# Kernel tuning notes

Measured on AMD Instinct MI355X. Metric: run time of the kernel, lower is better.

Reference implementation:

```python
import jax, jax.numpy as jnp
import numpy as np

B, D, K, H = 8192, 1024, 8, 2048


def setup_inputs() -> dict:
    key = jax.random.key(0)
    ks = jax.random.split(key, 4)
    x = jax.random.normal(ks[0], (B, D), dtype=jnp.float32)
    centroids = jax.random.normal(ks[1], (K, D), dtype=jnp.float32)
    W1 = jax.random.normal(ks[2], (K, D, H), dtype=jnp.float32) / np.sqrt(D).astype(np.float32)
    b1 = jnp.zeros((K, H), dtype=jnp.float32)
    W2 = jax.random.normal(ks[3], (K, H), dtype=jnp.float32) / np.sqrt(H).astype(np.float32)
    b2 = jnp.zeros((K,), dtype=jnp.float32)
    return {"x": x, "centroids": centroids, "W1": W1, "b1": b1, "W2": W2, "b2": b2}


def reference(x, centroids, W1, b1, W2, b2):
    # --- k-means hard routing: nearest centroid per sample (euclidean max_sim) ---
    # d2[b,k] = ||x_b||^2 - 2 x_b . c_k + ||c_k||^2  (avoid [B,K,D] blowup)
    d2 = (jnp.sum(x * x, axis=-1, keepdims=True)
          - 2.0 * (x @ centroids.T)
          + jnp.sum(centroids * centroids, axis=-1)[None, :])  # [B, K]
    cluster = jnp.argmin(d2, axis=-1)  # [B] int, hard assignment

    # --- per-expert log-likelihood heads (Einet stand-in), computed densely ---
    h = jnp.tanh(jnp.einsum("bd,kdh->kbh", x, W1) + b1[:, None, :])  # [K, B, H]
    lls = jnp.einsum("kbh,kh->kb", h, W2) + b2[:, None]              # [K, B]

    # --- combine: each sample takes the LL from its routed expert, original order ---
    lls_sorted = jnp.take_along_axis(lls.T, cluster[:, None], axis=1)[:, 0]  # [B]
    return lls_sorted
```

## Files before the change

### kernel.cpp

```cpp
#include <hip/hip_runtime.h>
#include <hip/hip_bf16.h>
#include <stdint.h>

#define B_N 8192
#define D_N 1024
#define K_N 8
#define H_N 2048

#define BM 320
#define BN 256
#define BK 64
#define NBLK 256
#define ABYTES 40960
#define BUFSZ 73728
#define RO_OFF 147456
#define PLL_OFF 148736
#define GEMM_LDS 153856

typedef unsigned int u32;
typedef unsigned short u16;
typedef __attribute__((ext_vector_type(8))) short short8;
typedef __attribute__((ext_vector_type(4))) float float4v;

struct __align__(8) us4 { u16 x, y, z, w; };

__device__ __forceinline__ u16 f2bf(float f) {
    union { float f; u32 u; } v; v.f = f;
    u32 u = v.u;
    u32 r = (u + 0x7fffu + ((u >> 16) & 1u)) >> 16;
    return (u16)r;
}

__device__ __forceinline__ float fast_tanh(float x) {
    float t = __expf(2.0f * x);
    return 1.0f - 2.0f * __builtin_amdgcn_rcpf(t + 1.0f);
}

__device__ __forceinline__ void async_copy16(void* lds, const void* g) {
    __builtin_amdgcn_global_load_lds(
        (const __attribute__((address_space(1))) void*)g,
        (__attribute__((address_space(3))) void*)lds, 16, 0, 0);
}

__global__ void route_kernel(const float* __restrict__ x,
                             const float* __restrict__ cent,
                             u16* __restrict__ xbf,
                             int* __restrict__ cluster,
                             u32* __restrict__ counts) {
    int tid = threadIdx.x;
    if (blockIdx.x == 0 && tid < K_N) counts[tid * 32] = 0;
    int wave = tid >> 6, lane = tid & 63;
    int b = blockIdx.x * 4 + wave;
    const float* xr = x + (size_t)b * D_N;

    float4 xv[4];
#pragma unroll
    for (int i = 0; i < 4; ++i)
        xv[i] = *(const float4*)(xr + i * 256 + lane * 4);

#pragma unroll
    for (int i = 0; i < 4; ++i) {
        us4 o;
        o.x = f2bf(xv[i].x); o.y = f2bf(xv[i].y);
        o.z = f2bf(xv[i].z); o.w = f2bf(xv[i].w);
        *(us4*)(xbf + (size_t)b * D_N + i * 256 + lane * 4) = o;
    }

    double acc[K_N];
#pragma unroll
    for (int k = 0; k < K_N; ++k) {
        const float* cr = cent + k * D_N;
        double s = 0.0;
#pragma unroll
        for (int i = 0; i < 4; ++i) {
            float4 cv = *(const float4*)(cr + i * 256 + lane * 4);
            double d0 = (double)xv[i].x - (double)cv.x; s += d0 * d0;
            double d1 = (double)xv[i].y - (double)cv.y; s += d1 * d1;
            double d2 = (double)xv[i].z - (double)cv.z; s += d2 * d2;
            double d3 = (double)xv[i].w - (double)cv.w; s += d3 * d3;
        }
        acc[k] = s;
    }
#pragma unroll
    for (int k = 0; k < K_N; ++k) {
        double v = acc[k];
        for (int off = 32; off; off >>= 1) v += __shfl_down(v, off);
        acc[k] = v;
    }
    if (lane == 0) {
        int best = 0; double bv = acc[0];
#pragma unroll
        for (int k = 1; k < K_N; ++k)
            if (acc[k] < bv) { bv = acc[k]; best = k; }
        cluster[b] = best;
    }
}

__global__ void scatter_kernel(const int* __restrict__ cluster,
                               u32* __restrict__ counts,
                               u32* __restrict__ idxl) {
    __shared__ u32 wcnt[4][K_N];
    __shared__ u32 gb[K_N];
    int tid = threadIdx.x;
    int b = blockIdx.x * 256 + tid;
    int lane = tid & 63, wid = tid >> 6;
    int cl = cluster[b];
    unsigned long long lower = (1ull << lane) - 1ull;
    u32 rank = 0;
#pragma unroll
    for (int k = 0; k < K_N; ++k) {
        unsigned long long mk = __ballot(cl == k);
        if (k == cl) rank = (u32)__popcll(mk & lower);
        if (lane == 0) wcnt[wid][k] = (u32)__popcll(mk);
    }
    __syncthreads();
    if (tid < K_N) {
        u32 tot = wcnt[0][tid] + wcnt[1][tid] + wcnt[2][tid] + wcnt[3][tid];
        gb[tid] = atomicAdd(&counts[tid * 32], tot);
    }
    __syncthreads();
    u32 woff = 0;
    if (wid > 0) woff += wcnt[0][cl];
    if (wid > 1) woff += wcnt[1][cl];
    if (wid > 2) woff += wcnt[2][cl];
    idxl[(size_t)cl * B_N + gb[cl] + woff + rank] = (u32)b;
}

__global__ void w1t_kernel(const float* __restrict__ w1, u16* __restrict__ w1t) {
    __shared__ float ts[64][65];
    int tid = threadIdx.x;
    int h0 = blockIdx.x * 64, d0 = blockIdx.y * 64, k = blockIdx.z;
    const float* src = w1 + ((size_t)k * D_N + d0) * H_N + h0;
#pragma unroll
    for (int i = 0; i < 4; ++i) {
        int q = i * 256 + tid;
        int r = q >> 4, c4 = (q & 15) * 4;
        float4 v = *(const float4*)(src + (size_t)r * H_N + c4);
        ts[c4 + 0][r] = v.x; ts[c4 + 1][r] = v.y;
        ts[c4 + 2][r] = v.z; ts[c4 + 3][r] = v.w;
    }
    __syncthreads();
    u16* dst = w1t + ((size_t)k * H_N + h0) * D_N + d0;
#pragma unroll
    for (int i = 0; i < 4; ++i) {
        int q = i * 256 + tid;
        int hr = q >> 4, d4 = (q & 15) * 4;
        us4 o;
        o.x = f2bf(ts[hr][d4 + 0]); o.y = f2bf(ts[hr][d4 + 1]);
        o.z = f2bf(ts[hr][d4 + 2]); o.w = f2bf(ts[hr][d4 + 3]);
        *(us4*)(dst + (size_t)hr * D_N + d4) = o;
    }
}

__global__ __launch_bounds__(512, 2) void gemm_kernel(
                            const u16* __restrict__ xbf,
                            const u16* __restrict__ w1t,
                            const float* __restrict__ b1,
                            const float* __restrict__ w2,
                            const u32* __restrict__ idxl,
                            const u32* __restrict__ counts,
                            float* __restrict__ llp) {
    extern __shared__ char lds[];
    int tid = threadIdx.x;
    int lane = tid & 63, w = tid >> 6;
    int wm = w >> 2, wn = w & 3;
    int wmbase = wm * 160;
    int l15 = lane & 15, l4 = lane >> 4;

    u32* ro = (u32*)(lds + RO_OFF);
    float* pll = (float*)(lds + PLL_OFF);

    int ntot = 0;
#pragma unroll
    for (int kk = 0; kk < K_N; ++kk)
        ntot += ((int)counts[kk * 32] + BM - 1) / BM;
    int total = ntot * 8;

    int swz = l15 & 7;
    u32 aB0 = (u32)((wmbase + l15) * 128 + (((0 + l4) ^ swz) << 4));
    u32 aB1 = (u32)((wmbase + l15) * 128 + (((4 + l4) ^ swz) << 4));
    u32 bB0 = (u32)(ABYTES + (wn * 64 + l15) * 128 + (((0 + l4) ^ swz) << 4));
    u32 bB1 = (u32)(ABYTES + (wn * 64 + l15) * 128 + (((4 + l4) ^ swz) << 4));

    const char* xb = (const char*)xbf;
    const char* wb = (const char*)w1t;

    for (int item = blockIdx.x; item < total; item += NBLK) {
        int tile = item >> 3, nc = item & 7;
        int k = 0, mt = 0, nt = 0;
#pragma unroll
        for (int kk = 0; kk < K_N; ++kk) {
            int c = (int)counts[kk * 32];
            int t = (c + BM - 1) / BM;
            if (tile >= nt && tile < nt + t) { k = kk; mt = tile - nt; }
            nt += t;
        }
        int cnt = (int)counts[k * 32];
        int rows = cnt - mt * BM; if (rows > BM) rows = BM;
        int h0 = nc * BN;

        if (tid < BM) {
            int m = mt * BM + tid;
            int mm = m < cnt ? m : cnt - 1;
            ro[tid] = idxl[(size_t)k * B_N + mm] * (u32)(D_N * 2);
        }
        __syncthreads();

        u32 srcA[5], srcB[4];
#pragma unroll
        for (int i = 0; i < 5; ++i) {
            int c = i * 512 + tid; int r = c >> 3, j = c & 7;
            srcA[i] = ro[r] + ((u32)(j ^ (r & 7)) << 4);
        }
#pragma unroll
        for (int i = 0; i < 4; ++i) {
            int c = i * 512 + tid; int r = c >> 3, j = c & 7;
            srcB[i] = ((u32)(k * H_N + h0 + r) << 11) + ((u32)(j ^ (r & 7)) << 4);
        }

        float4v acc[10][4];
#pragma unroll
        for (int mf = 0; mf < 10; ++mf)
#pragma unroll
            for (int nf = 0; nf < 4; ++nf)
                acc[mf][nf] = (float4v){0.f, 0.f, 0.f, 0.f};

#define STA(BUF, I, D) async_copy16((BUF) + (I) * 8192 + w * 1024, xb + srcA[I] + (D))
#define STB(BUF, I, D) async_copy16((BUF) + ABYTES + (I) * 8192 + w * 1024, wb + srcB[I] + (D))
#define BAR() do { asm volatile("" ::: "memory"); __builtin_amdgcn_s_barrier(); \
                   asm volatile("" ::: "memory"); } while (0)
#define LGKM0_PIN() do { asm volatile("s_waitcnt lgkmcnt(0)" ::: "memory"); \
                         __builtin_amdgcn_sched_barrier(0); } while (0)
#define MFMA_PHASE(MFB, BREG)                                                    \
    do {                                                                         \
        __builtin_amdgcn_s_setprio(1);                                           \
        _Pragma("unroll")                                                        \
        for (int i_ = 0; i_ < 5; ++i_) {                                         \
            if (wmbase + ((MFB) + i_) * 16 < rows) {                             \
                _Pragma("unroll")                                                \
                for (int nf_ = 0; nf_ < 4; ++nf_)                                \
                    acc[(MFB) + i_][nf_] = __builtin_amdgcn_mfma_f32_16x16x32_bf16( \
                        a[i_], BREG[nf_], acc[(MFB) + i_][nf_], 0, 0, 0);        \
            }                                                                    \
        }                                                                        \
        __builtin_amdgcn_s_setprio(0);                                           \
    } while (0)

        {
            char* Bp = lds;
            STA(Bp, 0, 0); STA(Bp, 1, 0); STA(Bp, 2, 0); STA(Bp, 3, 0); STA(Bp, 4, 0);
            STB(Bp, 0, 0); STB(Bp, 1, 0); STB(Bp, 2, 0); STB(Bp, 3, 0);
        }

        for (int t = 0; t < 16; ++t) {
            const char* Acur = lds + (t & 1) * BUFSZ;
            char* Bnx = lds + ((t + 1) & 1) * BUFSZ;
            u32 d = (u32)((t + 1) << 7);
            bool pre = (t < 15);
            short8 a[5], bC[4];

            asm volatile("s_waitcnt vmcnt(0)" ::: "memory");
            BAR();
#pragma unroll
            for (int nf = 0; nf < 4; ++nf)
                bC[nf] = *(const short8*)(Acur + bB0 + nf * 2048);
#pragma unroll
            for (int i = 0; i < 5; ++i)
                a[i] = *(const short8*)(Acur + aB0 + i * 2048);
            if (pre) { STB(Bnx, 0, d); STB(Bnx, 1, d); STB(Bnx, 2, d); }
            BAR();
            LGKM0_PIN();
            MFMA_PHASE(0, bC);

            BAR();
#pragma unroll
            for (int i = 0; i < 5; ++i)
                a[i] = *(const short8*)(Acur + aB0 + (5 + i) * 2048);
            if (pre) { STB(Bnx, 3, d); STA(Bnx, 0, d); STA(Bnx, 1, d); }
            BAR();
            LGKM0_PIN();
            MFMA_PHASE(5, bC);

            BAR();
#pragma unroll
            for (int nf = 0; nf < 4; ++nf)
                bC[nf] = *(const short8*)(Acur + bB1 + nf * 2048);
#pragma unroll
            for (int i = 0; i < 5; ++i)
                a[i] = *(const short8*)(Acur + aB1 + i * 2048);
            if (pre) { STA(Bnx, 2, d); STA(Bnx, 3, d); STA(Bnx, 4, d); }
            BAR();
            LGKM0_PIN();
            MFMA_PHASE(0, bC);

            BAR();
#pragma unroll
            for (int i = 0; i < 5; ++i)
                a[i] = *(const short8*)(Acur + aB1 + (5 + i) * 2048);
            BAR();
            LGKM0_PIN();
            MFMA_PHASE(5, bC);
        }

#undef STA
#undef STB
#undef BAR
#undef LGKM0_PIN
#undef MFMA_PHASE

        float w2v[4], b1v[4];
#pragma unroll
        for (int nf = 0; nf < 4; ++nf) {
            int h = h0 + wn * 64 + nf * 16 + l15;
            w2v[nf] = w2[k * H_N + h];
            b1v[nf] = b1[k * H_N + h];
        }
#pragma unroll
        for (int mf = 0; mf < 10; ++mf) {
            float rs[4] = {0.f, 0.f, 0.f, 0.f};
#pragma unroll
            for (int nf = 0; nf < 4; ++nf) {
#pragma unroll
                for (int r = 0; r < 4; ++r)
                    rs[r] += fast_tanh(acc[mf][nf][r] + b1v[nf]) * w2v[nf];
            }
#pragma unroll
            for (int r = 0; r < 4; ++r) {
                float v = rs[r];
                v += __shfl_xor(v, 8);
                v += __shfl_xor(v, 4);
                v += __shfl_xor(v, 2);
                v += __shfl_xor(v, 1);
                if (l15 == 0) pll[wn * 320 + wmbase + mf * 16 + l4 * 4 + r] = v;
            }
        }
        __syncthreads();
        if (tid < BM) {
            int m = mt * BM + tid;
            if (m < cnt) {
                u32 b = idxl[(size_t)k * B_N + m];
                llp[(size_t)nc * B_N + b] = pll[tid] + pll[320 + tid] + pll[640 + tid] + pll[960 + tid];
            }
        }
        __syncthreads();
    }
}

__global__ void combine_kernel(const float* __restrict__ llp,
                               const int* __restrict__ cluster,
                               const float* __restrict__ b2,
                               float* __restrict__ out) {
    int b = blockIdx.x * 256 + threadIdx.x;
    float s = b2[cluster[b]];
#pragma unroll
    for (int nc = 0; nc < 8; ++nc) s += llp[(size_t)nc * B_N + b];
    out[b] = s;
}

extern "C" void kernel_launch(void* const* d_in, const int* in_sizes, int n_in,
                              void* d_out, int out_size, void* d_ws, size_t ws_size,
                              hipStream_t stream) {
    const float* x    = (const float*)d_in[0];
    const float* cent = (const float*)d_in[1];
    const float* W1   = (const float*)d_in[2];
    const float* b1   = (const float*)d_in[3];
    const float* W2   = (const float*)d_in[4];
    const float* b2   = (const float*)d_in[5];
    float* out = (float*)d_out;

    char* ws = (char*)d_ws;
    u16* xbf     = (u16*)(ws + 0);
    u16* w1t     = (u16*)(ws + 16777216);
    u32* counts  = (u32*)(ws + 50331648);
    int* cluster = (int*)(ws + 50332672);
    u32* idxl    = (u32*)(ws + 50365440);
    float* llp   = (float*)(ws + 50627584);

    (void)hipFuncSetAttribute((const void*)gemm_kernel,
                              hipFuncAttributeMaxDynamicSharedMemorySize, GEMM_LDS);

    hipLaunchKernelGGL(route_kernel, dim3(B_N / 4), dim3(256), 0, stream,
                       x, cent, xbf, cluster, counts);
    hipLaunchKernelGGL(scatter_kernel, dim3(32), dim3(256), 0, stream,
                       cluster, counts, idxl);
    hipLaunchKernelGGL(w1t_kernel, dim3(H_N / 64, D_N / 64, K_N), dim3(256), 0, stream,
                       W1, w1t);
    hipLaunchKernelGGL(gemm_kernel, dim3(NBLK), dim3(512), GEMM_LDS, stream,
                       xbf, w1t, b1, W2, idxl, counts, llp);
    hipLaunchKernelGGL(combine_kernel, dim3(B_N / 256), dim3(256), 0, stream,
                       llp, cluster, b2, out);
}
```

Before: 88.53 us.

## Halve GEMM workgroup to four waves with 160x128 per-wave tiles

Shrinks the grouped GEMM workgroup from 8 waves to 4 waves, each computing a 160x128 output tile instead of 160x64. The goal is more register-level reuse of each A fragment across more B columns. It also replaces the four-phase barrier-interleaved schedule with one phase per K step: load all fragments, issue the next prefetch, run all MFMAs, then sync. The cost is a much larger per-thread footprint (80 accumulator fragments plus 36 operand vectors), which risks register spilling. Halving the waves per CU also gives less latency hiding and less overlap between copies and MFMAs.

Result: slower. 125.9 us (+42.2%).

```diff
diff --git a/kernel.cpp b/kernel.cpp
--- a/kernel.cpp
+++ b/kernel.cpp
@@ -15,7 +15,7 @@
 #define BUFSZ 73728
 #define RO_OFF 147456
 #define PLL_OFF 148736
-#define GEMM_LDS 153856
+#define GEMM_LDS 151296
 
 typedef unsigned int u32;
 typedef unsigned short u16;
@@ -152,7 +152,7 @@
     }
 }
 
-__global__ __launch_bounds__(512, 2) void gemm_kernel(
+__global__ __launch_bounds__(256, 1) void gemm_kernel(
                             const u16* __restrict__ xbf,
                             const u16* __restrict__ w1t,
                             const float* __restrict__ b1,
@@ -163,7 +163,7 @@
     extern __shared__ char lds[];
     int tid = threadIdx.x;
     int lane = tid & 63, w = tid >> 6;
-    int wm = w >> 2, wn = w & 3;
+    int wm = w >> 1, wn = w & 1;
     int wmbase = wm * 160;
     int l15 = lane & 15, l4 = lane >> 4;
 
@@ -179,8 +179,8 @@
     int swz = l15 & 7;
     u32 aB0 = (u32)((wmbase + l15) * 128 + (((0 + l4) ^ swz) << 4));
     u32 aB1 = (u32)((wmbase + l15) * 128 + (((4 + l4) ^ swz) << 4));
-    u32 bB0 = (u32)(ABYTES + (wn * 64 + l15) * 128 + (((0 + l4) ^ swz) << 4));
-    u32 bB1 = (u32)(ABYTES + (wn * 64 + l15) * 128 + (((4 + l4) ^ swz) << 4));
+    u32 bB0 = (u32)(ABYTES + (wn * 128 + l15) * 128 + (((0 + l4) ^ swz) << 4));
+    u32 bB1 = (u32)(ABYTES + (wn * 128 + l15) * 128 + (((4 + l4) ^ swz) << 4));
 
     const char* xb = (const char*)xbf;
     const char* wb = (const char*)w1t;
@@ -199,119 +199,99 @@
         int rows = cnt - mt * BM; if (rows > BM) rows = BM;
         int h0 = nc * BN;
 
-        if (tid < BM) {
-            int m = mt * BM + tid;
+#pragma unroll 2
+        for (int i = tid; i < BM; i += 256) {
+            int m = mt * BM + i;
             int mm = m < cnt ? m : cnt - 1;
-            ro[tid] = idxl[(size_t)k * B_N + mm] * (u32)(D_N * 2);
+            ro[i] = idxl[(size_t)k * B_N + mm] * (u32)(D_N * 2);
         }
         __syncthreads();
 
-        u32 srcA[5], srcB[4];
-#pragma unroll
-        for (int i = 0; i < 5; ++i) {
-            int c = i * 512 + tid; int r = c >> 3, j = c & 7;
+        u32 srcA[10], srcB[8];
+#pragma unroll
+        for (int i = 0; i < 10; ++i) {
+            int c = i * 256 + tid; int r = c >> 3, j = c & 7;
             srcA[i] = ro[r] + ((u32)(j ^ (r & 7)) << 4);
         }
 #pragma unroll
-        for (int i = 0; i < 4; ++i) {
-            int c = i * 512 + tid; int r = c >> 3, j = c & 7;
+        for (int i = 0; i < 8; ++i) {
+            int c = i * 256 + tid; int r = c >> 3, j = c & 7;
             srcB[i] = ((u32)(k * H_N + h0 + r) << 11) + ((u32)(j ^ (r & 7)) << 4);
         }
 
-        float4v acc[10][4];
+        float4v acc[10][8];
 #pragma unroll
         for (int mf = 0; mf < 10; ++mf)
 #pragma unroll
-            for (int nf = 0; nf < 4; ++nf)
+            for (int nf = 0; nf < 8; ++nf)
                 acc[mf][nf] = (float4v){0.f, 0.f, 0.f, 0.f};
-
-#define STA(BUF, I, D) async_copy16((BUF) + (I) * 8192 + w * 1024, xb + srcA[I] + (D))
-#define STB(BUF, I, D) async_copy16((BUF) + ABYTES + (I) * 8192 + w * 1024, wb + srcB[I] + (D))
-#define BAR() do { asm volatile("" ::: "memory"); __builtin_amdgcn_s_barrier(); \
-                   asm volatile("" ::: "memory"); } while (0)
-#define LGKM0_PIN() do { asm volatile("s_waitcnt lgkmcnt(0)" ::: "memory"); \
-                         __builtin_amdgcn_sched_barrier(0); } while (0)
-#define MFMA_PHASE(MFB, BREG)                                                    \
-    do {                                                                         \
-        __builtin_amdgcn_s_setprio(1);                                           \
-        _Pragma("unroll")                                                        \
-        for (int i_ = 0; i_ < 5; ++i_) {                                         \
-            if (wmbase + ((MFB) + i_) * 16 < rows) {                             \
-                _Pragma("unroll")                                                \
-                for (int nf_ = 0; nf_ < 4; ++nf_)                                \
-                    acc[(MFB) + i_][nf_] = __builtin_amdgcn_mfma_f32_16x16x32_bf16( \
-                        a[i_], BREG[nf_], acc[(MFB) + i_][nf_], 0, 0, 0);        \
-            }                                                                    \
-        }                                                                        \
-        __builtin_amdgcn_s_setprio(0);                                           \
-    } while (0)
 
         {
             char* Bp = lds;
-            STA(Bp, 0, 0); STA(Bp, 1, 0); STA(Bp, 2, 0); STA(Bp, 3, 0); STA(Bp, 4, 0);
-            STB(Bp, 0, 0); STB(Bp, 1, 0); STB(Bp, 2, 0); STB(Bp, 3, 0);
-        }
+#pragma unroll
+            for (int i = 0; i < 10; ++i)
+                async_copy16(Bp + i * 4096 + tid * 16, xb + srcA[i]);
+#pragma unroll
+            for (int i = 0; i < 8; ++i)
+                async_copy16(Bp + ABYTES + i * 4096 + tid * 16, wb + srcB[i]);
+        }
+        __syncthreads();
 
         for (int t = 0; t < 16; ++t) {
             const char* Acur = lds + (t & 1) * BUFSZ;
             char* Bnx = lds + ((t + 1) & 1) * BUFSZ;
             u32 d = (u32)((t + 1) << 7);
             bool pre = (t < 15);
-            short8 a[5], bC[4];
-
-            asm volatile("s_waitcnt vmcnt(0)" ::: "memory");
-            BAR();
-#pragma unroll
-            for (int nf = 0; nf < 4; ++nf)
-                bC[nf] = *(const short8*)(Acur + bB0 + nf * 2048);
-#pragma unroll
-            for (int i = 0; i < 5; ++i)
-                a[i] = *(const short8*)(Acur + aB0 + i * 2048);
-            if (pre) { STB(Bnx, 0, d); STB(Bnx, 1, d); STB(Bnx, 2, d); }
-            BAR();
-            LGKM0_PIN();
-            MFMA_PHASE(0, bC);
-
-            BAR();
-#pragma unroll
-            for (int i = 0; i < 5; ++i)
-                a[i] = *(const short8*)(Acur + aB0 + (5 + i) * 2048);
-            if (pre) { STB(Bnx, 3, d); STA(Bnx, 0, d); STA(Bnx, 1, d); }
-            BAR();
-            LGKM0_PIN();
-            MFMA_PHASE(5, bC);
-
-            BAR();
-#pragma unroll
-            for (int nf = 0; nf < 4; ++nf)
-                bC[nf] = *(const short8*)(Acur + bB1 + nf * 2048);
-#pragma unroll
-            for (int i = 0; i < 5; ++i)
-                a[i] = *(const short8*)(Acur + aB1 + i * 2048);
-            if (pre) { STA(Bnx, 2, d); STA(Bnx, 3, d); STA(Bnx, 4, d); }
-            BAR();
-            LGKM0_PIN();
-            MFMA_PHASE(0, bC);
-
-            BAR();
-#pragma unroll
-            for (int i = 0; i < 5; ++i)
-                a[i] = *(const short8*)(Acur + aB1 + (5 + i) * 2048);
-            BAR();
-            LGKM0_PIN();
-            MFMA_PHASE(5, bC);
-        }
-
-#undef STA
-#undef STB
-#undef BAR
-#undef LGKM0_PIN
-#undef MFMA_PHASE
-
-        float w2v[4], b1v[4];
-#pragma unroll
-        for (int nf = 0; nf < 4; ++nf) {
-            int h = h0 + wn * 64 + nf * 16 + l15;
+            short8 a0[10], a1[10], c0[8], c1[8];
+
+#pragma unroll
+            for (int nf = 0; nf < 8; ++nf)
+                c0[nf] = *(const short8*)(Acur + bB0 + nf * 2048);
+#pragma unroll
+            for (int mf = 0; mf < 10; ++mf)
+                a0[mf] = *(const short8*)(Acur + aB0 + mf * 2048);
+            if (pre) {
+#pragma unroll
+                for (int i = 0; i < 10; ++i)
+                    async_copy16(Bnx + i * 4096 + tid * 16, xb + srcA[i] + d);
+#pragma unroll
+                for (int i = 0; i < 8; ++i)
+                    async_copy16(Bnx + ABYTES + i * 4096 + tid * 16, wb + srcB[i] + d);
+            }
+#pragma unroll
+            for (int nf = 0; nf < 8; ++nf)
+                c1[nf] = *(const short8*)(Acur + bB1 + nf * 2048);
+#pragma unroll
+            for (int mf = 0; mf < 10; ++mf)
+                a1[mf] = *(const short8*)(Acur + aB1 + mf * 2048);
+
+            __builtin_amdgcn_s_setprio(1);
+#pragma unroll
+            for (int mf = 0; mf < 10; ++mf) {
+                if (wmbase + mf * 16 < rows) {
+#pragma unroll
+                    for (int nf = 0; nf < 8; ++nf)
+                        acc[mf][nf] = __builtin_amdgcn_mfma_f32_16x16x32_bf16(
+                            a0[mf], c0[nf], acc[mf][nf], 0, 0, 0);
+                }
+            }
+#pragma unroll
+            for (int mf = 0; mf < 10; ++mf) {
+                if (wmbase + mf * 16 < rows) {
+#pragma unroll
+                    for (int nf = 0; nf < 8; ++nf)
+                        acc[mf][nf] = __builtin_amdgcn_mfma_f32_16x16x32_bf16(
+                            a1[mf], c1[nf], acc[mf][nf], 0, 0, 0);
+                }
+            }
+            __builtin_amdgcn_s_setprio(0);
+            __syncthreads();
+        }
+
+        float w2v[8], b1v[8];
+#pragma unroll
+        for (int nf = 0; nf < 8; ++nf) {
+            int h = h0 + wn * 128 + nf * 16 + l15;
             w2v[nf] = w2[k * H_N + h];
             b1v[nf] = b1[k * H_N + h];
         }
@@ -319,7 +299,7 @@
         for (int mf = 0; mf < 10; ++mf) {
             float rs[4] = {0.f, 0.f, 0.f, 0.f};
 #pragma unroll
-            for (int nf = 0; nf < 4; ++nf) {
+            for (int nf = 0; nf < 8; ++nf) {
 #pragma unroll
                 for (int r = 0; r < 4; ++r)
                     rs[r] += fast_tanh(acc[mf][nf][r] + b1v[nf]) * w2v[nf];
@@ -335,11 +315,12 @@
             }
         }
         __syncthreads();
-        if (tid < BM) {
-            int m = mt * BM + tid;
+#pragma unroll 2
+        for (int i = tid; i < BM; i += 256) {
+            int m = mt * BM + i;
             if (m < cnt) {
                 u32 b = idxl[(size_t)k * B_N + m];
-                llp[(size_t)nc * B_N + b] = pll[tid] + pll[320 + tid] + pll[640 + tid] + pll[960 + tid];
+                llp[(size_t)nc * B_N + b] = pll[i] + pll[320 + i];
             }
         }
         __syncthreads();
@@ -385,7 +366,7 @@
                        cluster, counts, idxl);
     hipLaunchKernelGGL(w1t_kernel, dim3(H_N / 64, D_N / 64, K_N), dim3(256), 0, stream,
                        W1, w1t);
-    hipLaunchKernelGGL(gemm_kernel, dim3(NBLK), dim3(512), GEMM_LDS, stream,
+    hipLaunchKernelGGL(gemm_kernel, dim3(NBLK), dim3(256), GEMM_LDS, stream,
                        xbf, w1t, b1, W2, idxl, counts, llp);
     hipLaunchKernelGGL(combine_kernel, dim3(B_N / 256), dim3(256), 0, stream,
                        llp, cluster, b2, out);
```

## Halve GEMM tile to 160x128 with 256 threads and simplify pipeline

Applied to the files above, without the earlier changes.

Shrinks the grouped GEMM tile from 320x256 (8 waves) to 160x128 (4 waves), doubles the grid to 512 blocks and splits H into 16 column chunks instead of 8. The finely interleaved four-phase prefetch/barrier schedule is replaced by a simpler loop: issue the next stage's async copies, wait with vmcnt(9) for the current stage, then run two k-substeps of MFMAs. The goal is better load balance and occupancy on ragged per-cluster tiles. The cost is lower operand reuse per tile, more global traffic for the W1 and x tiles, and twice the partial-sum rows that combine_kernel has to read.

Result: slower. 95.87 us (+8.3%).

```diff
diff --git a/kernel.cpp b/kernel.cpp
--- a/kernel.cpp
+++ b/kernel.cpp
@@ -7,15 +7,15 @@
 #define K_N 8
 #define H_N 2048
 
-#define BM 320
-#define BN 256
+#define BM 160
+#define BN 128
 #define BK 64
-#define NBLK 256
-#define ABYTES 40960
-#define BUFSZ 73728
-#define RO_OFF 147456
-#define PLL_OFF 148736
-#define GEMM_LDS 153856
+#define NBLK 512
+#define ABYTES 20480
+#define BUFSZ 36864
+#define RO_OFF 73728
+#define PLL_OFF 74368
+#define GEMM_LDS 75648
 
 typedef unsigned int u32;
 typedef unsigned short u16;
@@ -152,7 +152,7 @@
     }
 }
 
-__global__ __launch_bounds__(512, 2) void gemm_kernel(
+__global__ __launch_bounds__(256, 2) void gemm_kernel(
                             const u16* __restrict__ xbf,
                             const u16* __restrict__ w1t,
                             const float* __restrict__ b1,
@@ -163,18 +163,18 @@
     extern __shared__ char lds[];
     int tid = threadIdx.x;
     int lane = tid & 63, w = tid >> 6;
-    int wm = w >> 2, wn = w & 3;
-    int wmbase = wm * 160;
+    int wm = w >> 1, wn = w & 1;
+    int wmbase = wm * 80;
     int l15 = lane & 15, l4 = lane >> 4;
 
     u32* ro = (u32*)(lds + RO_OFF);
     float* pll = (float*)(lds + PLL_OFF);
 
-    int ntot = 0;
+    int ntiles = 0;
 #pragma unroll
     for (int kk = 0; kk < K_N; ++kk)
-        ntot += ((int)counts[kk * 32] + BM - 1) / BM;
-    int total = ntot * 8;
+        ntiles += ((int)counts[kk * 32] + BM - 1) / BM;
+    int total = ntiles * 16;
 
     int swz = l15 & 7;
     u32 aB0 = (u32)((wmbase + l15) * 128 + (((0 + l4) ^ swz) << 4));
@@ -185,8 +185,12 @@
     const char* xb = (const char*)xbf;
     const char* wb = (const char*)w1t;
 
+#define BAR() do { asm volatile("" ::: "memory"); __builtin_amdgcn_s_barrier(); \
+                   asm volatile("" ::: "memory"); } while (0)
+
     for (int item = blockIdx.x; item < total; item += NBLK) {
-        int tile = item >> 3, nc = item & 7;
+        int nc = ((item & 7) << 1) | ((item >> 3) & 1);
+        int tile = item >> 4;
         int k = 0, mt = 0, nt = 0;
 #pragma unroll
         for (int kk = 0; kk < K_N; ++kk) {
@@ -209,104 +213,69 @@
         u32 srcA[5], srcB[4];
 #pragma unroll
         for (int i = 0; i < 5; ++i) {
-            int c = i * 512 + tid; int r = c >> 3, j = c & 7;
+            int c = i * 256 + tid; int r = c >> 3, j = c & 7;
             srcA[i] = ro[r] + ((u32)(j ^ (r & 7)) << 4);
         }
 #pragma unroll
         for (int i = 0; i < 4; ++i) {
-            int c = i * 512 + tid; int r = c >> 3, j = c & 7;
+            int c = i * 256 + tid; int r = c >> 3, j = c & 7;
             srcB[i] = ((u32)(k * H_N + h0 + r) << 11) + ((u32)(j ^ (r & 7)) << 4);
         }
 
-        float4v acc[10][4];
-#pragma unroll
-        for (int mf = 0; mf < 10; ++mf)
+        float4v acc[5][4];
+#pragma unroll
+        for (int mf = 0; mf < 5; ++mf)
 #pragma unroll
             for (int nf = 0; nf < 4; ++nf)
                 acc[mf][nf] = (float4v){0.f, 0.f, 0.f, 0.f};
 
-#define STA(BUF, I, D) async_copy16((BUF) + (I) * 8192 + w * 1024, xb + srcA[I] + (D))
-#define STB(BUF, I, D) async_copy16((BUF) + ABYTES + (I) * 8192 + w * 1024, wb + srcB[I] + (D))
-#define BAR() do { asm volatile("" ::: "memory"); __builtin_amdgcn_s_barrier(); \
-                   asm volatile("" ::: "memory"); } while (0)
-#define LGKM0_PIN() do { asm volatile("s_waitcnt lgkmcnt(0)" ::: "memory"); \
-                         __builtin_amdgcn_sched_barrier(0); } while (0)
-#define MFMA_PHASE(MFB, BREG)                                                    \
-    do {                                                                         \
-        __builtin_amdgcn_s_setprio(1);                                           \
-        _Pragma("unroll")                                                        \
-        for (int i_ = 0; i_ < 5; ++i_) {                                         \
-            if (wmbase + ((MFB) + i_) * 16 < rows) {                             \
-                _Pragma("unroll")                                                \
-                for (int nf_ = 0; nf_ < 4; ++nf_)                                \
-                    acc[(MFB) + i_][nf_] = __builtin_amdgcn_mfma_f32_16x16x32_bf16( \
-                        a[i_], BREG[nf_], acc[(MFB) + i_][nf_], 0, 0, 0);        \
-            }                                                                    \
-        }                                                                        \
-        __builtin_amdgcn_s_setprio(0);                                           \
-    } while (0)
-
-        {
-            char* Bp = lds;
-            STA(Bp, 0, 0); STA(Bp, 1, 0); STA(Bp, 2, 0); STA(Bp, 3, 0); STA(Bp, 4, 0);
-            STB(Bp, 0, 0); STB(Bp, 1, 0); STB(Bp, 2, 0); STB(Bp, 3, 0);
-        }
+#pragma unroll
+        for (int i = 0; i < 5; ++i)
+            async_copy16(lds + i * 4096 + tid * 16, xb + srcA[i]);
+#pragma unroll
+        for (int i = 0; i < 4; ++i)
+            async_copy16(lds + ABYTES + i * 4096 + tid * 16, wb + srcB[i]);
 
         for (int t = 0; t < 16; ++t) {
             const char* Acur = lds + (t & 1) * BUFSZ;
             char* Bnx = lds + ((t + 1) & 1) * BUFSZ;
-            u32 d = (u32)((t + 1) << 7);
-            bool pre = (t < 15);
-            short8 a[5], bC[4];
-
-            asm volatile("s_waitcnt vmcnt(0)" ::: "memory");
+            if (t < 15) {
+                u32 d = (u32)((t + 1) << 7);
+#pragma unroll
+                for (int i = 0; i < 5; ++i)
+                    async_copy16(Bnx + i * 4096 + tid * 16, xb + srcA[i] + d);
+#pragma unroll
+                for (int i = 0; i < 4; ++i)
+                    async_copy16(Bnx + ABYTES + i * 4096 + tid * 16, wb + srcB[i] + d);
+                asm volatile("s_waitcnt vmcnt(9)" ::: "memory");
+            } else {
+                asm volatile("s_waitcnt vmcnt(0)" ::: "memory");
+            }
             BAR();
 #pragma unroll
-            for (int nf = 0; nf < 4; ++nf)
-                bC[nf] = *(const short8*)(Acur + bB0 + nf * 2048);
-#pragma unroll
-            for (int i = 0; i < 5; ++i)
-                a[i] = *(const short8*)(Acur + aB0 + i * 2048);
-            if (pre) { STB(Bnx, 0, d); STB(Bnx, 1, d); STB(Bnx, 2, d); }
+            for (int kk = 0; kk < 2; ++kk) {
+                short8 bC[4], a[5];
+                u32 aB = kk ? aB1 : aB0, bB = kk ? bB1 : bB0;
+#pragma unroll
+                for (int nf = 0; nf < 4; ++nf)
+                    bC[nf] = *(const short8*)(Acur + bB + nf * 2048);
+#pragma unroll
+                for (int mf = 0; mf < 5; ++mf)
+                    a[mf] = *(const short8*)(Acur + aB + mf * 2048);
+                __builtin_amdgcn_s_setprio(1);
+#pragma unroll
+                for (int mf = 0; mf < 5; ++mf) {
+                    if (wmbase + mf * 16 < rows) {
+#pragma unroll
+                        for (int nf = 0; nf < 4; ++nf)
+                            acc[mf][nf] = __builtin_amdgcn_mfma_f32_16x16x32_bf16(
+                                a[mf], bC[nf], acc[mf][nf], 0, 0, 0);
+                    }
+                }
+                __builtin_amdgcn_s_setprio(0);
+            }
             BAR();
-            LGKM0_PIN();
-            MFMA_PHASE(0, bC);
-
-            BAR();
-#pragma unroll
-            for (int i = 0; i < 5; ++i)
-                a[i] = *(const short8*)(Acur + aB0 + (5 + i) * 2048);
-            if (pre) { STB(Bnx, 3, d); STA(Bnx, 0, d); STA(Bnx, 1, d); }
-            BAR();
-            LGKM0_PIN();
-            MFMA_PHASE(5, bC);
-
-            BAR();
-#pragma unroll
-            for (int nf = 0; nf < 4; ++nf)
-                bC[nf] = *(const short8*)(Acur + bB1 + nf * 2048);
-#pragma unroll
-            for (int i = 0; i < 5; ++i)
-                a[i] = *(const short8*)(Acur + aB1 + i * 2048);
-            if (pre) { STA(Bnx, 2, d); STA(Bnx, 3, d); STA(Bnx, 4, d); }
-            BAR();
-            LGKM0_PIN();
-            MFMA_PHASE(0, bC);
-
-            BAR();
-#pragma unroll
-            for (int i = 0; i < 5; ++i)
-                a[i] = *(const short8*)(Acur + aB1 + (5 + i) * 2048);
-            BAR();
-            LGKM0_PIN();
-            MFMA_PHASE(5, bC);
-        }
-
-#undef STA
-#undef STB
-#undef BAR
-#undef LGKM0_PIN
-#undef MFMA_PHASE
+        }
 
         float w2v[4], b1v[4];
 #pragma unroll
@@ -316,7 +285,7 @@
             b1v[nf] = b1[k * H_N + h];
         }
 #pragma unroll
-        for (int mf = 0; mf < 10; ++mf) {
+        for (int mf = 0; mf < 5; ++mf) {
             float rs[4] = {0.f, 0.f, 0.f, 0.f};
 #pragma unroll
             for (int nf = 0; nf < 4; ++nf) {
@@ -331,7 +300,7 @@
                 v += __shfl_xor(v, 4);
                 v += __shfl_xor(v, 2);
                 v += __shfl_xor(v, 1);
-                if (l15 == 0) pll[wn * 320 + wmbase + mf * 16 + l4 * 4 + r] = v;
+                if (l15 == 0) pll[wn * 160 + wmbase + mf * 16 + l4 * 4 + r] = v;
             }
         }
         __syncthreads();
@@ -339,11 +308,12 @@
             int m = mt * BM + tid;
             if (m < cnt) {
                 u32 b = idxl[(size_t)k * B_N + m];
-                llp[(size_t)nc * B_N + b] = pll[tid] + pll[320 + tid] + pll[640 + tid] + pll[960 + tid];
+                llp[(size_t)nc * B_N + b] = pll[tid] + pll[160 + tid];
             }
         }
         __syncthreads();
     }
+#undef BAR
 }
 
 __global__ void combine_kernel(const float* __restrict__ llp,
@@ -353,7 +323,7 @@
     int b = blockIdx.x * 256 + threadIdx.x;
     float s = b2[cluster[b]];
 #pragma unroll
-    for (int nc = 0; nc < 8; ++nc) s += llp[(size_t)nc * B_N + b];
+    for (int nc = 0; nc < 16; ++nc) s += llp[(size_t)nc * B_N + b];
     out[b] = s;
 }
 
@@ -385,7 +355,7 @@
                        cluster, counts, idxl);
     hipLaunchKernelGGL(w1t_kernel, dim3(H_N / 64, D_N / 64, K_N), dim3(256), 0, stream,
                        W1, w1t);
-    hipLaunchKernelGGL(gemm_kernel, dim3(NBLK), dim3(512), GEMM_LDS, stream,
+    hipLaunchKernelGGL(gemm_kernel, dim3(NBLK), dim3(256), GEMM_LDS, stream,
                        xbf, w1t, b1, W2, idxl, counts, llp);
     hipLaunchKernelGGL(combine_kernel, dim3(B_N / 256), dim3(256), 0, stream,
                        llp, cluster, b2, out);
```
